# Performance work log

Measured on AMD Instinct MI355X. Metric: run time of the kernel, lower is better.

The kernel has to match this reference:

```python
import jax, jax.numpy as jnp
import numpy as np

N = 10000
E = 160000
IN_DIM = 128
HID = 128
HEADS = 8
INT_DIM = 512
OUT_DIM = 3
NEG_SLOPE = 0.2


def gat_conv(x, src, dst, W, a_src, a_dst, b, heads, ch):
    # x: [N, F_in]; W: [F_in, heads*ch]; a_src/a_dst: [heads, ch]; b: [heads*ch]
    n = x.shape[0]
    h = (x @ W).reshape(n, heads, ch)                      # [N,H,C]
    alpha_src = jnp.einsum('nhc,hc->nh', h, a_src)         # [N,H]
    alpha_dst = jnp.einsum('nhc,hc->nh', h, a_dst)         # [N,H]
    e = jax.nn.leaky_relu(alpha_src[src] + alpha_dst[dst], NEG_SLOPE)  # [E,H]
    # segment softmax over incoming edges of each dst node
    emax = jax.ops.segment_max(e, dst, num_segments=n)     # [N,H]
    ee = jnp.exp(e - emax[dst])
    denom = jax.ops.segment_sum(ee, dst, num_segments=n)   # [N,H]
    alpha = ee / (denom[dst] + 1e-16)                      # [E,H]
    msg = h[src] * alpha[:, :, None]                       # [E,H,C]
    out = jax.ops.segment_sum(msg, dst, num_segments=n)    # [N,H,C]
    return out.reshape(n, heads * ch) + b


def setup_inputs() -> dict:
    key = jax.random.key(0)
    ks = jax.random.split(key, 20)

    def glorot(k, shape):
        fan = shape[0] + shape[-1]
        s = jnp.sqrt(6.0 / fan)
        return jax.random.uniform(k, shape, jnp.float32, -s, s)

    x = jax.random.normal(ks[0], (N, IN_DIM), jnp.float32)
    edge_index = jax.random.randint(ks[1], (2, E), 0, N, jnp.int32)
    return {
        'x': x,
        'edge_index': edge_index,
        'W1': glorot(ks[2], (IN_DIM, HEADS * HID)),
        'a_src1': glorot(ks[3], (HEADS, HID)),
        'a_dst1': glorot(ks[4], (HEADS, HID)),
        'b1': jnp.zeros((HEADS * HID,), jnp.float32),
        'W2': glorot(ks[5], (HEADS * HID, HEADS * HID)),
        'a_src2': glorot(ks[6], (HEADS, HID)),
        'a_dst2': glorot(ks[7], (HEADS, HID)),
        'b2': jnp.zeros((HEADS * HID,), jnp.float32),
        'W3': glorot(ks[8], (HEADS * HID, INT_DIM)),
        'a_src3': glorot(ks[9], (1, INT_DIM)),
        'a_dst3': glorot(ks[10], (1, INT_DIM)),
        'b3': jnp.zeros((INT_DIM,), jnp.float32),
        'Wl': glorot(ks[11], (INT_DIM, INT_DIM)),
        'bl': jnp.zeros((INT_DIM,), jnp.float32),
        'Wc': glorot(ks[12], (INT_DIM, OUT_DIM)),
        'bc': jnp.zeros((OUT_DIM,), jnp.float32),
    }


def reference(x, edge_index, W1, a_src1, a_dst1, b1, W2, a_src2, a_dst2, b2,
              W3, a_src3, a_dst3, b3, Wl, bl, Wc, bc):
    src, dst = edge_index[0], edge_index[1]
    # eval mode: dropout_edge and Dropout are identity
    h = gat_conv(x, src, dst, W1, a_src1, a_dst1, b1, HEADS, HID)
    h = jax.nn.relu(h)
    h = gat_conv(h, src, dst, W2, a_src2, a_dst2, b2, HEADS, HID)
    h = jax.nn.relu(h)
    h = gat_conv(h, src, dst, W3, a_src3, a_dst3, b3, 1, INT_DIM)
    h = jax.nn.relu(h)
    h = jax.nn.relu(h @ Wl + bl)
    return h @ Wc + bc
```

## Files before the change

### kernel.cpp

```cpp
#include <hip/hip_runtime.h>
#include <hip/hip_bf16.h>

#define NN 10000
#define EE 160000
#define IN_DIM 128
#define HID 128
#define HEADS 8
#define F1 (HEADS*HID)
#define INT_DIM 512
#define OUT_DIM 3
#define MPAD 10112

typedef __attribute__((ext_vector_type(8))) short bf16x8;
typedef __attribute__((ext_vector_type(4))) float f32x4;
typedef __attribute__((ext_vector_type(8))) _Float16 half8;
typedef __attribute__((ext_vector_type(4))) _Float16 half4;
typedef __attribute__((ext_vector_type(2))) _Float16 half2v;

#define WAVE_SYNC() do { asm volatile("s_waitcnt lgkmcnt(0)" ::: "memory"); \
                         __builtin_amdgcn_sched_barrier(0); } while(0)

__device__ inline short f2bf(float v){
    union { __hip_bfloat16 b; short s; } u;
    u.b = __float2bfloat16(v);
    return u.s;
}
__device__ inline float bf2f(short s){
    union { short s; __hip_bfloat16 b; } u;
    u.s = s;
    return __bfloat162float(u.b);
}

__global__ __launch_bounds__(256) void count_kernel(const int* __restrict__ dst, int E, int* __restrict__ cnt){
    int e = blockIdx.x*256 + threadIdx.x;
    if(e < E) atomicAdd(&cnt[dst[e]], 1);
}

__global__ __launch_bounds__(256) void scan_kernel(const int* __restrict__ cnt, int* __restrict__ rowp,
                                                   int* __restrict__ cursor, int n){
    __shared__ int sh[256];
    __shared__ int stotal;
    int t = threadIdx.x;
    if(t==0) stotal = 0;
    __syncthreads();
    for(int base=0; base<n; base+=256){
        int i = base + t;
        int v = (i<n) ? cnt[i] : 0;
        sh[t] = v;
        __syncthreads();
        #pragma unroll
        for(int off=1; off<256; off<<=1){
            int add = (t>=off) ? sh[t-off] : 0;
            __syncthreads();
            sh[t] += add;
            __syncthreads();
        }
        int excl = sh[t] - v;
        if(i<n){ rowp[i] = stotal + excl; cursor[i] = stotal + excl; }
        int chunk_total = sh[255];
        __syncthreads();
        if(t==0) stotal += chunk_total;
        __syncthreads();
    }
    if(t==0) rowp[n] = stotal;
}

__global__ __launch_bounds__(256) void fill_kernel(const int* __restrict__ src, const int* __restrict__ dst,
                                                   int E, int* __restrict__ cursor, int* __restrict__ colsrc){
    int e = blockIdx.x*256 + threadIdx.x;
    if(e < E){
        int d = dst[e];
        int pos = atomicAdd(&cursor[d], 1);
        colsrc[pos] = src[e];
    }
}

__global__ __launch_bounds__(256) void splitT_kernel(const float* __restrict__ B, short* __restrict__ Th,
                                                     short* __restrict__ Tl, int K, int N){
    __shared__ float tile[32][33];
    const int tx = threadIdx.x & 31, ty = threadIdx.x >> 5;
    const int n0 = blockIdx.x * 32, k0 = blockIdx.y * 32;
    #pragma unroll
    for(int i = 0; i < 32; i += 8)
        tile[ty + i][tx] = B[(size_t)(k0 + ty + i) * N + n0 + tx];
    __syncthreads();
    #pragma unroll
    for(int i = 0; i < 32; i += 8){
        int n = ty + i;
        float v = tile[tx][n];
        short hv = f2bf(v);
        Th[(size_t)(n0 + n) * K + k0 + tx] = hv;
        Tl[(size_t)(n0 + n) * K + k0 + tx] = f2bf(v - bf2f(hv));
    }
}

__global__ __launch_bounds__(256) void splitT16_kernel(const float* __restrict__ B, _Float16* __restrict__ T,
                                                       int K, int N){
    __shared__ float tile[32][33];
    const int tx = threadIdx.x & 31, ty = threadIdx.x >> 5;
    const int n0 = blockIdx.x * 32, k0 = blockIdx.y * 32;
    #pragma unroll
    for(int i = 0; i < 32; i += 8)
        tile[ty + i][tx] = B[(size_t)(k0 + ty + i) * N + n0 + tx];
    __syncthreads();
    #pragma unroll
    for(int i = 0; i < 32; i += 8){
        int n = ty + i;
        T[(size_t)(n0 + n) * K + k0 + tx] = (_Float16)tile[tx][n];
    }
}

__global__ __launch_bounds__(256) void aw1_kernel(const float* __restrict__ W1,
                                                  const float* __restrict__ a_src,
                                                  const float* __restrict__ a_dst,
                                                  float* __restrict__ aw){
    int idx = blockIdx.x*256 + threadIdx.x;
    if(idx >= 16*IN_DIM) return;
    int j = idx >> 7, k = idx & 127;
    int hj = j & 7;
    const float* av = (j < 8 ? a_src : a_dst) + hj*HID;
    const float* wr = W1 + (size_t)k*F1 + hj*HID;
    float s = 0.f;
    #pragma unroll 4
    for(int c = 0; c < HID; c++) s += av[c] * wr[c];
    aw[idx] = s;
}

__global__ __launch_bounds__(256) void alpha1_kernel(const float* __restrict__ x,
                                                     const float* __restrict__ aw,
                                                     float* __restrict__ asrc, float* __restrict__ adst){
    __shared__ float xs[16][128];
    __shared__ float aws[16][128];
    int t = threadIdx.x;
    int nb = blockIdx.x * 16;
    for(int i = t; i < 16*128; i += 256){
        xs[i >> 7][i & 127] = x[(size_t)nb*128 + i];
        aws[i >> 7][i & 127] = aw[i];
    }
    __syncthreads();
    int nl = t >> 4, j = t & 15;
    float s = 0.f;
    #pragma unroll 4
    for(int c = 0; c < 128; c++) s += xs[nl][c] * aws[j][c];
    int node = nb + nl;
    if(j < 8) asrc[node*8 + j] = s;
    else      adst[node*8 + (j-8)] = s;
}

__global__ __launch_bounds__(256) void agg1_kernel(const float* __restrict__ x,
                                                   const float* __restrict__ asrc,
                                                   const float* __restrict__ adst,
                                                   const int* __restrict__ rowp,
                                                   const int* __restrict__ colsrc,
                                                   _Float16* __restrict__ oa){
    const int w = threadIdx.x >> 6, l = threadIdx.x & 63;
    const int node = blockIdx.x*4 + w;
    __shared__ float sh_ee[4][64][8];
    int beg = rowp[node], end = rowp[node+1];
    float rd = adst[node*8 + (l & 7)];
    float acc0[8], acc1[8];
    #pragma unroll
    for(int h=0;h<8;h++){ acc0[h]=0.f; acc1[h]=0.f; }
    float dpart = 0.f;
    for(int base=beg; base<end; base+=64){
        int clen = min(64, end-base);
        WAVE_SYNC();
        int sreg = (l < clen) ? colsrc[base + l] : 0;
        for(int it=l; it<clen*8; it+=64){
            int j = it >> 3;
            int s = colsrc[base + j];
            float e = asrc[s*8 + (l & 7)] + rd;
            e = (e > 0.f) ? e : 0.2f*e;
            float ee = expf(e);
            sh_ee[w][j][l & 7] = ee;
            dpart += ee;
        }
        WAVE_SYNC();
        #pragma unroll 2
        for(int j=0;j<clen;j++){
            int s = __shfl(sreg, j);
            float2 xv = ((const float2*)(x + (size_t)s*128))[l];
            #pragma unroll
            for(int h=0;h<8;h++){
                float wt = sh_ee[w][j][h];
                acc0[h] += wt * xv.x;
                acc1[h] += wt * xv.y;
            }
        }
    }
    dpart += __shfl_xor(dpart, 8);
    dpart += __shfl_xor(dpart, 16);
    dpart += __shfl_xor(dpart, 32);
    #pragma unroll
    for(int h=0;h<8;h++){
        float dn = __shfl(dpart, h) + 1e-16f;
        half2v o = { (_Float16)(acc0[h]/dn), (_Float16)(acc1[h]/dn) };
        *(half2v*)(oa + (size_t)node*F1 + h*128 + 2*l) = o;
    }
}

__device__ inline void fma8x2(float* acc, half8 v0, half8 v1, float w0, float w1){
    #pragma unroll
    for(int k=0;k<8;k++){
        acc[k]   += w0 * (float)v0[k];
        acc[8+k] += w1 * (float)v1[k];
    }
}
__device__ inline void fma8(float* acc, half8 v, float w){
    #pragma unroll
    for(int k=0;k<8;k++) acc[k] += w * (float)v[k];
}

__global__ __launch_bounds__(256) void agg2_kernel(const _Float16* __restrict__ hbuf,
                                                   const float* __restrict__ asrc,
                                                   const float* __restrict__ adst,
                                                   const int* __restrict__ rowp,
                                                   const int* __restrict__ colsrc,
                                                   const float* __restrict__ bias,
                                                   _Float16* __restrict__ oa){
    const int w = threadIdx.x >> 6, l = threadIdx.x & 63;
    const int node = blockIdx.x*4 + w;
    __shared__ float sh_ee[4][64][8];
    int beg = rowp[node], end = rowp[node+1];
    float rd = adst[node*8 + (l & 7)];
    float acc[16];
    #pragma unroll
    for(int k=0;k<16;k++) acc[k]=0.f;
    float dpart = 0.f;
    for(int base=beg; base<end; base+=64){
        int clen = min(64, end-base);
        WAVE_SYNC();
        int sreg = (l < clen) ? colsrc[base + l] : 0;
        #pragma unroll 1
        for(int it=l; it<512; it+=64){
            int j = it >> 3;
            float ee = 0.f;
            if(j < clen){
                int s = colsrc[base + j];
                float e = asrc[s*8 + (l & 7)] + rd;
                e = (e > 0.f) ? e : 0.2f*e;
                ee = expf(e);
                dpart += ee;
            }
            sh_ee[w][j][l & 7] = ee;
        }
        WAVE_SYNC();
        int cpad = (clen + 3) & ~3;
        int sA=__shfl(sreg,0), sB=__shfl(sreg,1), sC=__shfl(sreg,2), sD=__shfl(sreg,3);
        const half8* pA=(const half8*)(hbuf+(size_t)sA*F1);
        const half8* pB=(const half8*)(hbuf+(size_t)sB*F1);
        const half8* pC=(const half8*)(hbuf+(size_t)sC*F1);
        const half8* pD=(const half8*)(hbuf+(size_t)sD*F1);
        half8 vA0=pA[l], vA1=pA[l+64];
        half8 vB0=pB[l], vB1=pB[l+64];
        half8 vC0=pC[l], vC1=pC[l+64];
        half8 vD0=pD[l], vD1=pD[l+64];
        const int h0 = l>>4, h1 = 4 + (l>>4);
        #pragma unroll 1
        for(int j0=0; j0<cpad; j0+=4){
            half8 nA0,nA1,nB0,nB1,nC0,nC1,nD0,nD1;
            const bool more = (j0+4 < cpad);
            if(more){
                int t0=__shfl(sreg,j0+4), t1=__shfl(sreg,j0+5), t2=__shfl(sreg,j0+6), t3=__shfl(sreg,j0+7);
                const half8* q0=(const half8*)(hbuf+(size_t)t0*F1);
                const half8* q1=(const half8*)(hbuf+(size_t)t1*F1);
                const half8* q2=(const half8*)(hbuf+(size_t)t2*F1);
                const half8* q3=(const half8*)(hbuf+(size_t)t3*F1);
                nA0=q0[l]; nA1=q0[l+64];
                nB0=q1[l]; nB1=q1[l+64];
                nC0=q2[l]; nC1=q2[l+64];
                nD0=q3[l]; nD1=q3[l+64];
            }
            fma8x2(acc, vA0, vA1, sh_ee[w][j0  ][h0], sh_ee[w][j0  ][h1]);
            fma8x2(acc, vB0, vB1, sh_ee[w][j0+1][h0], sh_ee[w][j0+1][h1]);
            fma8x2(acc, vC0, vC1, sh_ee[w][j0+2][h0], sh_ee[w][j0+2][h1]);
            fma8x2(acc, vD0, vD1, sh_ee[w][j0+3][h0], sh_ee[w][j0+3][h1]);
            if(more){
                vA0=nA0; vA1=nA1; vB0=nB0; vB1=nB1;
                vC0=nC0; vC1=nC1; vD0=nD0; vD1=nD1;
            }
        }
    }
    dpart += __shfl_xor(dpart, 8);
    dpart += __shfl_xor(dpart, 16);
    dpart += __shfl_xor(dpart, 32);
    float dn0 = __shfl(dpart, l>>4) + 1e-16f;
    float dn1 = __shfl(dpart, 4 + (l>>4)) + 1e-16f;
    const float4* bp = (const float4*)bias;
    float4 ba0 = bp[2*l],       ba1 = bp[2*l+1];
    float4 bc0 = bp[128 + 2*l], bc1 = bp[128 + 2*l+1];
    float bb0[8] = {ba0.x,ba0.y,ba0.z,ba0.w, ba1.x,ba1.y,ba1.z,ba1.w};
    float bb1[8] = {bc0.x,bc0.y,bc0.z,bc0.w, bc1.x,bc1.y,bc1.z,bc1.w};
    half8 o0, o1;
    #pragma unroll
    for(int k=0;k<8;k++){
        o0[k] = (_Float16)fmaxf(acc[k]/dn0 + bb0[k], 0.f);
        o1[k] = (_Float16)fmaxf(acc[8+k]/dn1 + bb1[k], 0.f);
    }
    size_t off0 = (size_t)node*F1 + 8*l;
    *(half8*)(oa + off0) = o0;
    *(half8*)(oa + off0 + 512) = o1;
}

__global__ __launch_bounds__(256) void agg3_kernel(const _Float16* __restrict__ hbuf,
                                                   const float* __restrict__ asrc,
                                                   const float* __restrict__ adst,
                                                   const int* __restrict__ rowp,
                                                   const int* __restrict__ colsrc,
                                                   const float* __restrict__ bias,
                                                   short* __restrict__ oh, short* __restrict__ ol){
    const int w = threadIdx.x >> 6, l = threadIdx.x & 63;
    const int node = blockIdx.x*4 + w;
    int beg = rowp[node], end = rowp[node+1];
    float rd = adst[node];
    float acc[8];
    #pragma unroll
    for(int k=0;k<8;k++) acc[k]=0.f;
    float dpart = 0.f;
    for(int base=beg; base<end; base+=64){
        int clen = min(64, end-base);
        int sreg = 0; float eereg = 0.f;
        if(l < clen){
            sreg = colsrc[base + l];
            float e = asrc[sreg] + rd;
            e = (e > 0.f) ? e : 0.2f*e;
            eereg = expf(e);
            dpart += eereg;
        }
        int cpad = (clen + 7) & ~7;
        half8 v[8];
        float wt[8];
        #pragma unroll
        for(int k=0;k<8;k++){
            int s = __shfl(sreg, k);
            wt[k] = __shfl(eereg, k);
            v[k] = ((const half8*)(hbuf + (size_t)s*INT_DIM))[l];
        }
        #pragma unroll 1
        for(int j0=0; j0<cpad; j0+=8){
            half8 nv[8]; float nw[8];
            const bool more = (j0+8 < cpad);
            if(more){
                #pragma unroll
                for(int k=0;k<8;k++){
                    int s = __shfl(sreg, j0+8+k);
                    nw[k] = __shfl(eereg, j0+8+k);
                    nv[k] = ((const half8*)(hbuf + (size_t)s*INT_DIM))[l];
                }
            }
            #pragma unroll
            for(int k=0;k<8;k++) fma8(acc, v[k], wt[k]);
            if(more){
                #pragma unroll
                for(int k=0;k<8;k++){ v[k]=nv[k]; wt[k]=nw[k]; }
            }
        }
    }
    #pragma unroll
    for(int off=1; off<64; off<<=1) dpart += __shfl_xor(dpart, off);
    float dn = dpart + 1e-16f;
    const float4* bp = (const float4*)bias;
    float4 ba0 = bp[2*l], ba1 = bp[2*l+1];
    float bb[8] = {ba0.x,ba0.y,ba0.z,ba0.w, ba1.x,ba1.y,ba1.z,ba1.w};
    bf16x8 hi, lo;
    #pragma unroll
    for(int k=0;k<8;k++){
        float vv = fmaxf(acc[k]/dn + bb[k], 0.f);
        short hv = f2bf(vv); hi[k]=hv; lo[k]=f2bf(vv - bf2f(hv));
    }
    size_t o = (size_t)node*INT_DIM + 8*l;
    *(bf16x8*)(oh + o) = hi;
    *(bf16x8*)(ol + o) = lo;
}

template<int FUSE>
__global__ __launch_bounds__(512, 4) void mfma16_gemm_kernel(
    const _Float16* __restrict__ A, int lda, int za,
    const _Float16* __restrict__ B, int ldb, int zb,
    const float* __restrict__ bias, _Float16* __restrict__ O,
    int ldc, int zc, int K, int gx)
{
    __shared__ _Float16 lA[2][128*32];
    __shared__ _Float16 lB[2][128*32];
    const int tid  = threadIdx.x;
    const int lane = tid & 63;
    const int w    = tid >> 6;
    const int wm   = w >> 2;
    const int wn   = w & 3;
    const int z    = blockIdx.z;

    const int nwg = gridDim.x;
    const int q = nwg >> 3, r = nwg & 7;
    const int xcd = blockIdx.x & 7, idx = blockIdx.x >> 3;
    const int wgid = (xcd < r ? xcd*(q+1) : r*(q+1) + (xcd-r)*q) + idx;
    const int row0 = (wgid / gx) * 128, col0 = (wgid % gx) * 128;

    f32x4 acc[4][2];
    #pragma unroll
    for(int i=0;i<4;i++)
        #pragma unroll
        for(int j=0;j<2;j++) acc[i][j] = (f32x4){0.f,0.f,0.f,0.f};

    const int rr1 = tid >> 2;
    const int ss1 = (tid & 3) ^ ((rr1 >> 1) & 3);
    const size_t aoff = (size_t)(row0 + rr1) * lda + (size_t)z*za + ss1 * 8;
    const size_t boff = (size_t)(col0 + rr1) * ldb + (size_t)z*zb + ss1 * 8;

    typedef __attribute__((address_space(3))) char lds_char;
    lds_char* dA = (lds_char*)(&lA[0][0]) + w*1024;
    lds_char* dB = (lds_char*)(&lB[0][0]) + w*1024;

    int arow[4], brow[2];
    const int slotx = ((lane >> 4) ^ ((lane >> 1) & 3)) << 4;
    #pragma unroll
    for(int i=0;i<4;i++)
        arow[i] = (wm*64 + i*16 + (lane & 15)) * 64 + slotx;
    #pragma unroll
    for(int j=0;j<2;j++)
        brow[j] = (wn*32 + j*16 + (lane & 15)) * 64 + slotx;

    #define GLDS(src, dst) __builtin_amdgcn_global_load_lds( \
        (__attribute__((address_space(1))) void*)(src), \
        (__attribute__((address_space(3))) void*)(dst), 16, 0, 0)
    GLDS(A + aoff, dA);
    GLDS(B + boff, dB);
    __syncthreads();

    #pragma unroll 1
    for(int k0 = 0, kb = 0; k0 < K; k0 += 32, kb ^= 1){
        if(k0 + 32 < K){
            const int nb = kb ^ 1;
            GLDS(A + aoff + k0 + 32, dA + nb*8192);
            GLDS(B + boff + k0 + 32, dB + nb*8192);
        }
        const char* pA = (const char*)(&lA[0][0]) + kb*8192;
        const char* pB = (const char*)(&lB[0][0]) + kb*8192;
        half8 af[4];
        #pragma unroll
        for(int i=0;i<4;i++) af[i] = *(const half8*)(pA + arow[i]);
        #pragma unroll
        for(int j=0;j<2;j++){
            half8 bf = *(const half8*)(pB + brow[j]);
            #pragma unroll
            for(int i=0;i<4;i++)
                acc[i][j] = __builtin_amdgcn_mfma_f32_16x16x32_f16(af[i], bf, acc[i][j], 0, 0, 0);
        }
        __syncthreads();
    }
    #undef GLDS

    #pragma unroll
    for(int i=0;i<4;i++){
        const int rr = row0 + wm*64 + i*16 + ((lane >> 4) << 2);
        #pragma unroll
        for(int j=0;j<2;j++){
            const int gc = z*zc + col0 + wn*32 + j*16 + (lane & 15);
            float b = FUSE ? bias[gc] : 0.f;
            #pragma unroll
            for(int rg=0;rg<4;rg++){
                float v = acc[i][j][rg];
                if(FUSE) v = fmaxf(v + b, 0.f);
                O[(size_t)(rr + rg) * ldc + gc] = (_Float16)v;
            }
        }
    }
}

__global__ __launch_bounds__(512, 4) void mfma_gemm_kernel(
    const short* __restrict__ Ah, const short* __restrict__ Al, int lda,
    const short* __restrict__ Bh, const short* __restrict__ Bl, int ldb,
    const float* __restrict__ bias, float* __restrict__ C,
    int ldc, int K, int gx)
{
    __shared__ short lAh[2][128*32];
    __shared__ short lAl[2][128*32];
    __shared__ short lBh[2][128*32];
    __shared__ short lBl[2][128*32];
    const int tid  = threadIdx.x;
    const int lane = tid & 63;
    const int w    = tid >> 6;
    const int wm   = w >> 2;
    const int wn   = w & 3;

    const int nwg = gridDim.x;
    const int q = nwg >> 3, r = nwg & 7;
    const int xcd = blockIdx.x & 7, idx = blockIdx.x >> 3;
    const int wgid = (xcd < r ? xcd*(q+1) : r*(q+1) + (xcd-r)*q) + idx;
    const int row0 = (wgid / gx) * 128, col0 = (wgid % gx) * 128;

    f32x4 acc[4][2];
    #pragma unroll
    for(int i=0;i<4;i++)
        #pragma unroll
        for(int j=0;j<2;j++) acc[i][j] = (f32x4){0.f,0.f,0.f,0.f};

    const int rr1 = tid >> 2;
    const int ss1 = (tid & 3) ^ ((rr1 >> 1) & 3);
    const size_t aoff = (size_t)(row0 + rr1) * lda + ss1 * 8;
    const size_t boff = (size_t)(col0 + rr1) * ldb + ss1 * 8;

    typedef __attribute__((address_space(3))) char lds_char;
    lds_char* dAh = (lds_char*)(&lAh[0][0]) + w*1024;
    lds_char* dAl = (lds_char*)(&lAl[0][0]) + w*1024;
    lds_char* dBh = (lds_char*)(&lBh[0][0]) + w*1024;
    lds_char* dBl = (lds_char*)(&lBl[0][0]) + w*1024;

    int arow[4], brow[2];
    const int slotx = ((lane >> 4) ^ ((lane >> 1) & 3)) << 4;
    #pragma unroll
    for(int i=0;i<4;i++)
        arow[i] = (wm*64 + i*16 + (lane & 15)) * 64 + slotx;
    #pragma unroll
    for(int j=0;j<2;j++)
        brow[j] = (wn*32 + j*16 + (lane & 15)) * 64 + slotx;

    #define GLDS(src, dst) __builtin_amdgcn_global_load_lds( \
        (__attribute__((address_space(1))) void*)(src), \
        (__attribute__((address_space(3))) void*)(dst), 16, 0, 0)
    GLDS(Ah + aoff, dAh);
    GLDS(Al + aoff, dAl);
    GLDS(Bh + boff, dBh);
    GLDS(Bl + boff, dBl);
    __syncthreads();

    #pragma unroll 1
    for(int k0 = 0, kb = 0; k0 < K; k0 += 32, kb ^= 1){
        if(k0 + 32 < K){
            const int nb = kb ^ 1;
            GLDS(Ah + aoff + k0 + 32, dAh + nb*8192);
            GLDS(Al + aoff + k0 + 32, dAl + nb*8192);
            GLDS(Bh + boff + k0 + 32, dBh + nb*8192);
            GLDS(Bl + boff + k0 + 32, dBl + nb*8192);
        }
        const char* pAh = (const char*)(&lAh[0][0]) + kb*8192;
        const char* pAl = (const char*)(&lAl[0][0]) + kb*8192;
        const char* pBh = (const char*)(&lBh[0][0]) + kb*8192;
        const char* pBl = (const char*)(&lBl[0][0]) + kb*8192;
        bf16x8 afh[4], afl[4];
        #pragma unroll
        for(int i=0;i<4;i++){
            afh[i] = *(const bf16x8*)(pAh + arow[i]);
            afl[i] = *(const bf16x8*)(pAl + arow[i]);
        }
        #pragma unroll
        for(int j=0;j<2;j++){
            bf16x8 bh = *(const bf16x8*)(pBh + brow[j]);
            bf16x8 bl = *(const bf16x8*)(pBl + brow[j]);
            #pragma unroll
            for(int i=0;i<4;i++){
                acc[i][j] = __builtin_amdgcn_mfma_f32_16x16x32_bf16(afh[i], bh, acc[i][j], 0, 0, 0);
                acc[i][j] = __builtin_amdgcn_mfma_f32_16x16x32_bf16(afh[i], bl, acc[i][j], 0, 0, 0);
                acc[i][j] = __builtin_amdgcn_mfma_f32_16x16x32_bf16(afl[i], bh, acc[i][j], 0, 0, 0);
            }
        }
        __syncthreads();
    }
    #undef GLDS

    #pragma unroll
    for(int i=0;i<4;i++){
        const int rr = row0 + wm*64 + i*16 + ((lane >> 4) << 2);
        #pragma unroll
        for(int j=0;j<2;j++){
            const int gc = col0 + wn*32 + j*16 + (lane & 15);
            float b = bias[gc];
            #pragma unroll
            for(int rg=0;rg<4;rg++){
                float v = fmaxf(acc[i][j][rg] + b, 0.f);
                C[(size_t)(rr + rg) * ldc + gc] = v;
            }
        }
    }
}

__global__ __launch_bounds__(128) void alpha16_h8_kernel(const _Float16* __restrict__ hbuf,
                                                         const float* __restrict__ a_src,
                                                         const float* __restrict__ a_dst,
                                                         float* __restrict__ asrc, float* __restrict__ adst){
    int node = blockIdx.x;
    int t = threadIdx.x;
    half8 v = ((const half8*)(hbuf + (size_t)node*F1))[t];
    const float4* ap = (const float4*)(a_src + 8*t);
    const float4* dp = (const float4*)(a_dst + 8*t);
    float4 a0 = ap[0], a1 = ap[1];
    float4 d0 = dp[0], d1 = dp[1];
    float av[8] = {a0.x,a0.y,a0.z,a0.w, a1.x,a1.y,a1.z,a1.w};
    float dv[8] = {d0.x,d0.y,d0.z,d0.w, d1.x,d1.y,d1.z,d1.w};
    float ps = 0.f, pd = 0.f;
    #pragma unroll
    for(int k=0;k<8;k++){
        float f = (float)v[k];
        ps += f * av[k];
        pd += f * dv[k];
    }
    #pragma unroll
    for(int off=8; off; off>>=1){ ps += __shfl_down(ps, off); pd += __shfl_down(pd, off); }
    if((t & 15) == 0){
        asrc[(size_t)node*8 + (t>>4)] = ps;
        adst[(size_t)node*8 + (t>>4)] = pd;
    }
}

__global__ __launch_bounds__(128) void alpha16_h1_kernel(const _Float16* __restrict__ hbuf,
                                                         const float* __restrict__ a_src,
                                                         const float* __restrict__ a_dst,
                                                         float* __restrict__ asrc, float* __restrict__ adst){
    int node = blockIdx.x;
    int t = threadIdx.x;
    half4 v = ((const half4*)(hbuf + (size_t)node*INT_DIM))[t];
    float4 a = ((const float4*)a_src)[t];
    float4 d = ((const float4*)a_dst)[t];
    float ps = (float)v[0]*a.x + (float)v[1]*a.y + (float)v[2]*a.z + (float)v[3]*a.w;
    float pd = (float)v[0]*d.x + (float)v[1]*d.y + (float)v[2]*d.z + (float)v[3]*d.w;
    #pragma unroll
    for(int off=32; off; off>>=1){ ps += __shfl_down(ps, off); pd += __shfl_down(pd, off); }
    __shared__ float shs[2], shd[2];
    int wv = t >> 6;
    if((t & 63) == 0){ shs[wv] = ps; shd[wv] = pd; }
    __syncthreads();
    if(t == 0){
        asrc[node] = shs[0] + shs[1];
        adst[node] = shd[0] + shd[1];
    }
}

__global__ __launch_bounds__(256) void cls_kernel(const float* __restrict__ h, const float* __restrict__ Wc,
                                                  const float* __restrict__ bc, float* __restrict__ out, int n){
    int node = blockIdx.x*4 + (threadIdx.x >> 6);
    int lane = threadIdx.x & 63;
    if(node >= n) return;
    float s0=0.f, s1=0.f, s2=0.f;
    const float* hr = h + (size_t)node*INT_DIM;
    for(int k=lane; k<INT_DIM; k+=64){
        float v = hr[k];
        s0 += v * Wc[k*3+0];
        s1 += v * Wc[k*3+1];
        s2 += v * Wc[k*3+2];
    }
    #pragma unroll
    for(int off=32; off; off>>=1){
        s0 += __shfl_down(s0, off);
        s1 += __shfl_down(s1, off);
        s2 += __shfl_down(s2, off);
    }
    if(lane==0){
        out[(size_t)node*3+0] = s0 + bc[0];
        out[(size_t)node*3+1] = s1 + bc[1];
        out[(size_t)node*3+2] = s2 + bc[2];
    }
}

extern "C" void kernel_launch(void* const* d_in, const int* in_sizes, int n_in,
                              void* d_out, int out_size, void* d_ws, size_t ws_size,
                              hipStream_t stream){
    const float* x      = (const float*)d_in[0];
    const int*   ei     = (const int*)d_in[1];
    const float* W1     = (const float*)d_in[2];
    const float* a_src1 = (const float*)d_in[3];
    const float* a_dst1 = (const float*)d_in[4];
    const float* b1     = (const float*)d_in[5];
    const float* W2     = (const float*)d_in[6];
    const float* a_src2 = (const float*)d_in[7];
    const float* a_dst2 = (const float*)d_in[8];
    const float* b2     = (const float*)d_in[9];
    const float* W3     = (const float*)d_in[10];
    const float* a_src3 = (const float*)d_in[11];
    const float* a_dst3 = (const float*)d_in[12];
    const float* b3     = (const float*)d_in[13];
    const float* Wl     = (const float*)d_in[14];
    const float* bl     = (const float*)d_in[15];
    const float* Wc     = (const float*)d_in[16];
    const float* bc     = (const float*)d_in[17];
    float* out = (float*)d_out;

    const int* src = ei;
    const int* dst = ei + EE;

    char* p = (char*)d_ws;
    char* regA = p;  p += (size_t)MPAD*F1*4;
    char* regB = p;  p += (size_t)MPAD*F1*4;
    short* wt_h = (short*)p;  p += (size_t)F1*F1*2;
    short* wt_l = (short*)p;  p += (size_t)F1*F1*2;
    float* aw1  = (float*)p;  p += 16*IN_DIM*4;
    float* asrc = (float*)p;  p += (size_t)NN*HEADS*4;
    float* adst = (float*)p;  p += (size_t)NN*HEADS*4;
    int* cnt    = (int*)p;    p += NN*4;
    int* rowp   = (int*)p;    p += (NN+1)*4;
    int* cursor = (int*)p;    p += NN*4;
    int* colsrc = (int*)p;    p += EE*4;

    _Float16* hA = (_Float16*)regA;
    _Float16* hB = (_Float16*)regB;
    float* Af = (float*)regA;
    short* qh = (short*)regB;  short* ql = qh + (size_t)MPAD*INT_DIM;
    _Float16* wt16 = (_Float16*)wt_h;

    hipMemsetAsync(cnt, 0, NN*sizeof(int), stream);
    count_kernel<<<(EE+255)/256, 256, 0, stream>>>(dst, EE, cnt);
    scan_kernel<<<1, 256, 0, stream>>>(cnt, rowp, cursor, NN);
    fill_kernel<<<(EE+255)/256, 256, 0, stream>>>(src, dst, EE, cursor, colsrc);

    splitT16_kernel<<<dim3(F1/32, IN_DIM/32), 256, 0, stream>>>(W1, wt16, IN_DIM, F1);
    aw1_kernel<<<8, 256, 0, stream>>>(W1, a_src1, a_dst1, aw1);
    alpha1_kernel<<<NN/16, 256, 0, stream>>>(x, aw1, asrc, adst);
    agg1_kernel<<<NN/4, 256, 0, stream>>>(x, asrc, adst, rowp, colsrc, hA);
    mfma16_gemm_kernel<1><<<dim3(MPAD/128, 1, HEADS), 512, 0, stream>>>(
        hA, F1, 128,  wt16, IN_DIM, 128*IN_DIM,
        b1, hB, F1, 128,  IN_DIM, 1);

    splitT16_kernel<<<dim3(F1/32, F1/32), 256, 0, stream>>>(W2, wt16, F1, F1);
    mfma16_gemm_kernel<0><<<dim3((F1/128)*(MPAD/128), 1, 1), 512, 0, stream>>>(
        hB, F1, 0,  wt16, F1, 0,
        nullptr, hA, F1, 0,  F1, F1/128);
    alpha16_h8_kernel<<<NN, 128, 0, stream>>>(hA, a_src2, a_dst2, asrc, adst);
    agg2_kernel<<<NN/4, 256, 0, stream>>>(hA, asrc, adst, rowp, colsrc, b2, hB);

    splitT16_kernel<<<dim3(INT_DIM/32, F1/32), 256, 0, stream>>>(W3, wt16, F1, INT_DIM);
    mfma16_gemm_kernel<0><<<dim3((INT_DIM/128)*(MPAD/128), 1, 1), 512, 0, stream>>>(
        hB, F1, 0,  wt16, F1, 0,
        nullptr, hA, INT_DIM, 0,  F1, INT_DIM/128);
    alpha16_h1_kernel<<<NN, 128, 0, stream>>>(hA, a_src3, a_dst3, asrc, adst);
    agg3_kernel<<<NN/4, 256, 0, stream>>>(hA, asrc, adst, rowp, colsrc, b3, qh, ql);

    splitT_kernel<<<dim3(INT_DIM/32, INT_DIM/32), 256, 0, stream>>>(Wl, wt_h, wt_l, INT_DIM, INT_DIM);
    mfma_gemm_kernel<<<dim3((INT_DIM/128)*(MPAD/128), 1, 1), 512, 0, stream>>>(
        qh, ql, INT_DIM,  wt_h, wt_l, INT_DIM,
        bl, Af, INT_DIM,  INT_DIM, INT_DIM/128);

    cls_kernel<<<(NN+3)/4, 256, 0, stream>>>(Af, Wc, bc, out, NN);
}
```

Before: 306.5 us.

## Use fp16 for the final linear layer and the layer-1 feature gather

Replaces the split-bf16 (hi/lo, three MFMAs per step) GEMM for the final linear layer with the existing single-pass fp16 MFMA GEMM. agg3 now writes fp16 activations and the classifier reads fp16. Input x is converted to fp16 once so agg1 gathers half the bytes per neighbor, and agg2's softmax-weight loop is bounded by the padded chunk length instead of a fixed 512. This cuts memory traffic and MFMA work at the cost of precision in the last layers.

```diff
diff --git a/kernel.cpp b/kernel.cpp
--- a/kernel.cpp
+++ b/kernel.cpp
@@ -11,7 +11,6 @@
 #define OUT_DIM 3
 #define MPAD 10112
 
-typedef __attribute__((ext_vector_type(8))) short bf16x8;
 typedef __attribute__((ext_vector_type(4))) float f32x4;
 typedef __attribute__((ext_vector_type(8))) _Float16 half8;
 typedef __attribute__((ext_vector_type(4))) _Float16 half4;
@@ -19,17 +18,6 @@
 
 #define WAVE_SYNC() do { asm volatile("s_waitcnt lgkmcnt(0)" ::: "memory"); \
                          __builtin_amdgcn_sched_barrier(0); } while(0)
-
-__device__ inline short f2bf(float v){
-    union { __hip_bfloat16 b; short s; } u;
-    u.b = __float2bfloat16(v);
-    return u.s;
-}
-__device__ inline float bf2f(short s){
-    union { short s; __hip_bfloat16 b; } u;
-    u.s = s;
-    return __bfloat162float(u.b);
-}
 
 __global__ __launch_bounds__(256) void count_kernel(const int* __restrict__ dst, int E, int* __restrict__ cnt){
     int e = blockIdx.x*256 + threadIdx.x;
@@ -75,25 +63,6 @@
     }
 }
 
-__global__ __launch_bounds__(256) void splitT_kernel(const float* __restrict__ B, short* __restrict__ Th,
-                                                     short* __restrict__ Tl, int K, int N){
-    __shared__ float tile[32][33];
-    const int tx = threadIdx.x & 31, ty = threadIdx.x >> 5;
-    const int n0 = blockIdx.x * 32, k0 = blockIdx.y * 32;
-    #pragma unroll
-    for(int i = 0; i < 32; i += 8)
-        tile[ty + i][tx] = B[(size_t)(k0 + ty + i) * N + n0 + tx];
-    __syncthreads();
-    #pragma unroll
-    for(int i = 0; i < 32; i += 8){
-        int n = ty + i;
-        float v = tile[tx][n];
-        short hv = f2bf(v);
-        Th[(size_t)(n0 + n) * K + k0 + tx] = hv;
-        Tl[(size_t)(n0 + n) * K + k0 + tx] = f2bf(v - bf2f(hv));
-    }
-}
-
 __global__ __launch_bounds__(256) void splitT16_kernel(const float* __restrict__ B, _Float16* __restrict__ T,
                                                        int K, int N){
     __shared__ float tile[32][33];
@@ -108,6 +77,14 @@
         int n = ty + i;
         T[(size_t)(n0 + n) * K + k0 + tx] = (_Float16)tile[tx][n];
     }
+}
+
+__global__ __launch_bounds__(256) void x16_kernel(const float* __restrict__ x, _Float16* __restrict__ x16, int n4){
+    int i = blockIdx.x*256 + threadIdx.x;
+    if(i >= n4) return;
+    float4 v = ((const float4*)x)[i];
+    half4 o = { (_Float16)v.x, (_Float16)v.y, (_Float16)v.z, (_Float16)v.w };
+    ((half4*)x16)[i] = o;
 }
 
 __global__ __launch_bounds__(256) void aw1_kernel(const float* __restrict__ W1,
@@ -147,7 +124,7 @@
     else      adst[node*8 + (j-8)] = s;
 }
 
-__global__ __launch_bounds__(256) void agg1_kernel(const float* __restrict__ x,
+__global__ __launch_bounds__(256) void agg1_kernel(const _Float16* __restrict__ x16,
                                                    const float* __restrict__ asrc,
                                                    const float* __restrict__ adst,
                                                    const int* __restrict__ rowp,
@@ -179,12 +156,13 @@
         #pragma unroll 2
         for(int j=0;j<clen;j++){
             int s = __shfl(sreg, j);
-            float2 xv = ((const float2*)(x + (size_t)s*128))[l];
+            half2v xv = ((const half2v*)(x16 + (size_t)s*128))[l];
+            float x0 = (float)xv[0], x1 = (float)xv[1];
             #pragma unroll
             for(int h=0;h<8;h++){
                 float wt = sh_ee[w][j][h];
-                acc0[h] += wt * xv.x;
-                acc1[h] += wt * xv.y;
+                acc0[h] += wt * x0;
+                acc1[h] += wt * x1;
             }
         }
     }
@@ -229,10 +207,11 @@
     float dpart = 0.f;
     for(int base=beg; base<end; base+=64){
         int clen = min(64, end-base);
+        int cpad = (clen + 3) & ~3;
         WAVE_SYNC();
         int sreg = (l < clen) ? colsrc[base + l] : 0;
         #pragma unroll 1
-        for(int it=l; it<512; it+=64){
+        for(int it=l; it<cpad*8; it+=64){
             int j = it >> 3;
             float ee = 0.f;
             if(j < clen){
@@ -245,7 +224,6 @@
             sh_ee[w][j][l & 7] = ee;
         }
         WAVE_SYNC();
-        int cpad = (clen + 3) & ~3;
         int sA=__shfl(sreg,0), sB=__shfl(sreg,1), sC=__shfl(sreg,2), sD=__shfl(sreg,3);
         const half8* pA=(const half8*)(hbuf+(size_t)sA*F1);
         const half8* pB=(const half8*)(hbuf+(size_t)sB*F1);
@@ -308,7 +286,7 @@
                                                    const int* __restrict__ rowp,
                                                    const int* __restrict__ colsrc,
                                                    const float* __restrict__ bias,
-                                                   short* __restrict__ oh, short* __restrict__ ol){
+                                                   _Float16* __restrict__ oa){
     const int w = threadIdx.x >> 6, l = threadIdx.x & 63;
     const int node = blockIdx.x*4 + w;
     int beg = rowp[node], end = rowp[node+1];
@@ -362,15 +340,11 @@
     const float4* bp = (const float4*)bias;
     float4 ba0 = bp[2*l], ba1 = bp[2*l+1];
     float bb[8] = {ba0.x,ba0.y,ba0.z,ba0.w, ba1.x,ba1.y,ba1.z,ba1.w};
-    bf16x8 hi, lo;
-    #pragma unroll
-    for(int k=0;k<8;k++){
-        float vv = fmaxf(acc[k]/dn + bb[k], 0.f);
-        short hv = f2bf(vv); hi[k]=hv; lo[k]=f2bf(vv - bf2f(hv));
-    }
-    size_t o = (size_t)node*INT_DIM + 8*l;
-    *(bf16x8*)(oh + o) = hi;
-    *(bf16x8*)(ol + o) = lo;
+    half8 o;
+    #pragma unroll
+    for(int k=0;k<8;k++)
+        o[k] = (_Float16)fmaxf(acc[k]/dn + bb[k], 0.f);
+    *(half8*)(oa + (size_t)node*INT_DIM + 8*l) = o;
 }
 
 template<int FUSE>
@@ -466,113 +440,6 @@
     }
 }
 
-__global__ __launch_bounds__(512, 4) void mfma_gemm_kernel(
-    const short* __restrict__ Ah, const short* __restrict__ Al, int lda,
-    const short* __restrict__ Bh, const short* __restrict__ Bl, int ldb,
-    const float* __restrict__ bias, float* __restrict__ C,
-    int ldc, int K, int gx)
-{
-    __shared__ short lAh[2][128*32];
-    __shared__ short lAl[2][128*32];
-    __shared__ short lBh[2][128*32];
-    __shared__ short lBl[2][128*32];
-    const int tid  = threadIdx.x;
-    const int lane = tid & 63;
-    const int w    = tid >> 6;
-    const int wm   = w >> 2;
-    const int wn   = w & 3;
-
-    const int nwg = gridDim.x;
-    const int q = nwg >> 3, r = nwg & 7;
-    const int xcd = blockIdx.x & 7, idx = blockIdx.x >> 3;
-    const int wgid = (xcd < r ? xcd*(q+1) : r*(q+1) + (xcd-r)*q) + idx;
-    const int row0 = (wgid / gx) * 128, col0 = (wgid % gx) * 128;
-
-    f32x4 acc[4][2];
-    #pragma unroll
-    for(int i=0;i<4;i++)
-        #pragma unroll
-        for(int j=0;j<2;j++) acc[i][j] = (f32x4){0.f,0.f,0.f,0.f};
-
-    const int rr1 = tid >> 2;
-    const int ss1 = (tid & 3) ^ ((rr1 >> 1) & 3);
-    const size_t aoff = (size_t)(row0 + rr1) * lda + ss1 * 8;
-    const size_t boff = (size_t)(col0 + rr1) * ldb + ss1 * 8;
-
-    typedef __attribute__((address_space(3))) char lds_char;
-    lds_char* dAh = (lds_char*)(&lAh[0][0]) + w*1024;
-    lds_char* dAl = (lds_char*)(&lAl[0][0]) + w*1024;
-    lds_char* dBh = (lds_char*)(&lBh[0][0]) + w*1024;
-    lds_char* dBl = (lds_char*)(&lBl[0][0]) + w*1024;
-
-    int arow[4], brow[2];
-    const int slotx = ((lane >> 4) ^ ((lane >> 1) & 3)) << 4;
-    #pragma unroll
-    for(int i=0;i<4;i++)
-        arow[i] = (wm*64 + i*16 + (lane & 15)) * 64 + slotx;
-    #pragma unroll
-    for(int j=0;j<2;j++)
-        brow[j] = (wn*32 + j*16 + (lane & 15)) * 64 + slotx;
-
-    #define GLDS(src, dst) __builtin_amdgcn_global_load_lds( \
-        (__attribute__((address_space(1))) void*)(src), \
-        (__attribute__((address_space(3))) void*)(dst), 16, 0, 0)
-    GLDS(Ah + aoff, dAh);
-    GLDS(Al + aoff, dAl);
-    GLDS(Bh + boff, dBh);
-    GLDS(Bl + boff, dBl);
-    __syncthreads();
-
-    #pragma unroll 1
-    for(int k0 = 0, kb = 0; k0 < K; k0 += 32, kb ^= 1){
-        if(k0 + 32 < K){
-            const int nb = kb ^ 1;
-            GLDS(Ah + aoff + k0 + 32, dAh + nb*8192);
-            GLDS(Al + aoff + k0 + 32, dAl + nb*8192);
-            GLDS(Bh + boff + k0 + 32, dBh + nb*8192);
-            GLDS(Bl + boff + k0 + 32, dBl + nb*8192);
-        }
-        const char* pAh = (const char*)(&lAh[0][0]) + kb*8192;
-        const char* pAl = (const char*)(&lAl[0][0]) + kb*8192;
-        const char* pBh = (const char*)(&lBh[0][0]) + kb*8192;
-        const char* pBl = (const char*)(&lBl[0][0]) + kb*8192;
-        bf16x8 afh[4], afl[4];
-        #pragma unroll
-        for(int i=0;i<4;i++){
-            afh[i] = *(const bf16x8*)(pAh + arow[i]);
-            afl[i] = *(const bf16x8*)(pAl + arow[i]);
-        }
-        #pragma unroll
-        for(int j=0;j<2;j++){
-            bf16x8 bh = *(const bf16x8*)(pBh + brow[j]);
-            bf16x8 bl = *(const bf16x8*)(pBl + brow[j]);
-            #pragma unroll
-            for(int i=0;i<4;i++){
-                acc[i][j] = __builtin_amdgcn_mfma_f32_16x16x32_bf16(afh[i], bh, acc[i][j], 0, 0, 0);
-                acc[i][j] = __builtin_amdgcn_mfma_f32_16x16x32_bf16(afh[i], bl, acc[i][j], 0, 0, 0);
-                acc[i][j] = __builtin_amdgcn_mfma_f32_16x16x32_bf16(afl[i], bh, acc[i][j], 0, 0, 0);
-            }
-        }
-        __syncthreads();
-    }
-    #undef GLDS
-
-    #pragma unroll
-    for(int i=0;i<4;i++){
-        const int rr = row0 + wm*64 + i*16 + ((lane >> 4) << 2);
-        #pragma unroll
-        for(int j=0;j<2;j++){
-            const int gc = col0 + wn*32 + j*16 + (lane & 15);
-            float b = bias[gc];
-            #pragma unroll
-            for(int rg=0;rg<4;rg++){
-                float v = fmaxf(acc[i][j][rg] + b, 0.f);
-                C[(size_t)(rr + rg) * ldc + gc] = v;
-            }
-        }
-    }
-}
-
 __global__ __launch_bounds__(128) void alpha16_h8_kernel(const _Float16* __restrict__ hbuf,
                                                          const float* __restrict__ a_src,
                                                          const float* __restrict__ a_dst,
@@ -624,18 +491,20 @@
     }
 }
 
-__global__ __launch_bounds__(256) void cls_kernel(const float* __restrict__ h, const float* __restrict__ Wc,
-                                                  const float* __restrict__ bc, float* __restrict__ out, int n){
+__global__ __launch_bounds__(256) void cls16_kernel(const _Float16* __restrict__ h, const float* __restrict__ Wc,
+                                                    const float* __restrict__ bc, float* __restrict__ out, int n){
     int node = blockIdx.x*4 + (threadIdx.x >> 6);
     int lane = threadIdx.x & 63;
     if(node >= n) return;
+    half8 v = ((const half8*)(h + (size_t)node*INT_DIM))[lane];
     float s0=0.f, s1=0.f, s2=0.f;
-    const float* hr = h + (size_t)node*INT_DIM;
-    for(int k=lane; k<INT_DIM; k+=64){
-        float v = hr[k];
-        s0 += v * Wc[k*3+0];
-        s1 += v * Wc[k*3+1];
-        s2 += v * Wc[k*3+2];
+    #pragma unroll
+    for(int k=0;k<8;k++){
+        float f = (float)v[k];
+        const float* wr = Wc + (8*lane + k)*3;
+        s0 += f * wr[0];
+        s1 += f * wr[1];
+        s2 += f * wr[2];
     }
     #pragma unroll
     for(int off=32; off; off>>=1){
@@ -679,8 +548,8 @@
     char* p = (char*)d_ws;
     char* regA = p;  p += (size_t)MPAD*F1*4;
     char* regB = p;  p += (size_t)MPAD*F1*4;
-    short* wt_h = (short*)p;  p += (size_t)F1*F1*2;
-    short* wt_l = (short*)p;  p += (size_t)F1*F1*2;
+    _Float16* wt16 = (_Float16*)p;  p += (size_t)F1*F1*2;
+    _Float16* x16  = (_Float16*)p;  p += (size_t)NN*IN_DIM*2;
     float* aw1  = (float*)p;  p += 16*IN_DIM*4;
     float* asrc = (float*)p;  p += (size_t)NN*HEADS*4;
     float* adst = (float*)p;  p += (size_t)NN*HEADS*4;
@@ -691,19 +560,17 @@
 
     _Float16* hA = (_Float16*)regA;
     _Float16* hB = (_Float16*)regB;
-    float* Af = (float*)regA;
-    short* qh = (short*)regB;  short* ql = qh + (size_t)MPAD*INT_DIM;
-    _Float16* wt16 = (_Float16*)wt_h;
 
     hipMemsetAsync(cnt, 0, NN*sizeof(int), stream);
     count_kernel<<<(EE+255)/256, 256, 0, stream>>>(dst, EE, cnt);
     scan_kernel<<<1, 256, 0, stream>>>(cnt, rowp, cursor, NN);
     fill_kernel<<<(EE+255)/256, 256, 0, stream>>>(src, dst, EE, cursor, colsrc);
 
+    x16_kernel<<<(NN*IN_DIM/4 + 255)/256, 256, 0, stream>>>(x, x16, NN*IN_DIM/4);
     splitT16_kernel<<<dim3(F1/32, IN_DIM/32), 256, 0, stream>>>(W1, wt16, IN_DIM, F1);
     aw1_kernel<<<8, 256, 0, stream>>>(W1, a_src1, a_dst1, aw1);
     alpha1_kernel<<<NN/16, 256, 0, stream>>>(x, aw1, asrc, adst);
-    agg1_kernel<<<NN/4, 256, 0, stream>>>(x, asrc, adst, rowp, colsrc, hA);
+    agg1_kernel<<<NN/4, 256, 0, stream>>>(x16, asrc, adst, rowp, colsrc, hA);
     mfma16_gemm_kernel<1><<<dim3(MPAD/128, 1, HEADS), 512, 0, stream>>>(
         hA, F1, 128,  wt16, IN_DIM, 128*IN_DIM,
         b1, hB, F1, 128,  IN_DIM, 1);
@@ -720,12 +587,12 @@
         hB, F1, 0,  wt16, F1, 0,
         nullptr, hA, INT_DIM, 0,  F1, INT_DIM/128);
     alpha16_h1_kernel<<<NN, 128, 0, stream>>>(hA, a_src3, a_dst3, asrc, adst);
-    agg3_kernel<<<NN/4, 256, 0, stream>>>(hA, asrc, adst, rowp, colsrc, b3, qh, ql);
-
-    splitT_kernel<<<dim3(INT_DIM/32, INT_DIM/32), 256, 0, stream>>>(Wl, wt_h, wt_l, INT_DIM, INT_DIM);
-    mfma_gemm_kernel<<<dim3((INT_DIM/128)*(MPAD/128), 1, 1), 512, 0, stream>>>(
-        qh, ql, INT_DIM,  wt_h, wt_l, INT_DIM,
-        bl, Af, INT_DIM,  INT_DIM, INT_DIM/128);
-
-    cls_kernel<<<(NN+3)/4, 256, 0, stream>>>(Af, Wc, bc, out, NN);
-}
+    agg3_kernel<<<NN/4, 256, 0, stream>>>(hA, asrc, adst, rowp, colsrc, b3, hB);
+
+    splitT16_kernel<<<dim3(INT_DIM/32, INT_DIM/32), 256, 0, stream>>>(Wl, wt16, INT_DIM, INT_DIM);
+    mfma16_gemm_kernel<1><<<dim3((INT_DIM/128)*(MPAD/128), 1, 1), 512, 0, stream>>>(
+        hB, INT_DIM, 0,  wt16, INT_DIM, 0,
+        bl, hA, INT_DIM, 0,  INT_DIM, INT_DIM/128);
+
+    cls16_kernel<<<(NN+3)/4, 256, 0, stream>>>(hA, Wc, bc, out, NN);
+}
```

Result: faster. 297.5 us (-2.9%).
